# Optimization experiments

Hardware: AMD Instinct MI355X
Metric: run time of the kernel (lower is better)

The kernel has to match this reference:

```python
import jax, jax.numpy as jnp
import numpy as np

B, S, N, F, H = 128, 128, 24, 16, 32  # batch, seq, nodes, in-feat/node, hid/node


def setup_inputs() -> dict:
    key = jax.random.key(0)
    ks = jax.random.split(key, 7)
    IS, HS = N * F, N * H
    stdv = 1.0 / np.sqrt(HS).astype(np.float32)
    x = jax.random.normal(ks[0], (B, S, N, F), jnp.float32)
    h0 = jax.random.normal(ks[1], (B, N, H), jnp.float32)
    c0 = jax.random.normal(ks[2], (B, N, H), jnp.float32)
    G = jax.random.normal(ks[3], (N, N), jnp.float32)
    W = jax.random.uniform(ks[4], (IS, 4 * HS), jnp.float32, -stdv, stdv)
    U = jax.random.uniform(ks[5], (HS, 4 * HS), jnp.float32, -stdv, stdv)
    bias = jax.random.uniform(ks[6], (4 * HS,), jnp.float32, -stdv, stdv)
    return {"x": x, "h0": h0, "c0": c0, "W": W, "U": U, "bias": bias, "G": G}


def _graph_masks(G, F, H):
    # repeat_interleave(G, r, dim=-2) == kron(G, ones(r,1)); dim=-1 == kron(G, ones(1,c)).
    # Then tile x4 along last dim for the 4 LSTM gates.
    GW = jnp.tile(jnp.kron(G, jnp.ones((F, H), G.dtype)), (1, 4))  # [N*F, 4*N*H]
    GU = jnp.tile(jnp.kron(G, jnp.ones((H, H), G.dtype)), (1, 4))  # [N*H, 4*N*H]
    return GW, GU


def reference(x, h0, c0, W, U, bias, G):
    B, S, N, F = x.shape
    H = h0.shape[-1]
    HS = N * H
    GW, GU = _graph_masks(G, F, H)
    Wm = W * GW                      # masked input weights
    Um = U * GU                      # masked recurrent weights
    # Non-recurrent term batched into one big GEMM over all timesteps.
    xf = x.reshape(B, S, N * F)
    xg = jnp.einsum('bsi,ig->bsg', xf, Wm) + bias  # [B,S,4*HS]
    h = h0.reshape(B, HS)
    c = c0.reshape(B, HS)

    def step(carry, xg_t):
        h, c = carry
        gates = xg_t + h @ Um
        i = jax.nn.sigmoid(gates[:, :HS])
        f = jax.nn.sigmoid(gates[:, HS:2 * HS])
        g = jnp.tanh(gates[:, 2 * HS:3 * HS])
        o = jax.nn.sigmoid(gates[:, 3 * HS:])
        c = f * c + i * g
        h = o * jnp.tanh(c)
        return (h, c), h

    (h, c), hs = jax.lax.scan(step, (h, c), jnp.swapaxes(xg, 0, 1))  # hs: [S,B,HS]
    hidden_seq = jnp.swapaxes(hs, 0, 1).reshape(B, S, N, H)
    return hidden_seq, (h.reshape(B, N, H), c.reshape(B, N, H))
```

## Files before the change

### kernel.cpp

```cpp
#include <hip/hip_runtime.h>
#include <hip/hip_bf16.h>


typedef __bf16 bf16x8 __attribute__((ext_vector_type(8)));
typedef float f32x4 __attribute__((ext_vector_type(4)));

#define HS 768
#define GATES 3072
#define KV 1152
#define SEQ 128
#define BATCH 128
#define OUT_HID (BATCH*SEQ*HS)
#define LROW 2352
#define XOFF 768
#define NWG 192
#define TEAM_WGS 24

__device__ __forceinline__ float fast_sig(float x) {
    return 1.0f / (1.0f + __expf(-x));
}
__device__ __forceinline__ float fast_tanh(float x) {
    x = fminf(fmaxf(x, -15.0f), 15.0f);
    float e = __expf(2.0f * x);
    return (e - 1.0f) / (e + 1.0f);
}

__device__ __forceinline__ bf16x8 cvt8(const float* src) {
    float4 v0 = *(const float4*)src;
    float4 v1 = *(const float4*)(src + 4);
    bf16x8 p;
    p[0] = (__bf16)v0.x; p[1] = (__bf16)v0.y; p[2] = (__bf16)v0.z; p[3] = (__bf16)v0.w;
    p[4] = (__bf16)v1.x; p[5] = (__bf16)v1.y; p[6] = (__bf16)v1.z; p[7] = (__bf16)v1.w;
    return p;
}

__global__ void prep_kernel(const float* __restrict__ W, const float* __restrict__ U,
                            const float* __restrict__ G, __bf16* __restrict__ VmT) {
    __shared__ __bf16 tile[64][65];
    const int kvb = blockIdx.x * 64;
    const int cb  = blockIdx.y * 64;
    const int tid = threadIdx.x;
    {
        const int cl = tid & 63, kl0 = tid >> 6;
        #pragma unroll
        for (int i = 0; i < 16; ++i) {
            int kl = kl0 + i * 4;
            int kv = kvb + kl;
            int c  = cb + cl;
            int nout = (c % HS) >> 5;
            float g, v;
            if (kv < 384) {
                g = G[(kv >> 4) * 24 + nout];
                v = W[(size_t)kv * GATES + c];
            } else {
                int ku = kv - 384;
                g = G[(ku >> 5) * 24 + nout];
                v = U[(size_t)ku * GATES + c];
            }
            tile[kl][cl] = (__bf16)(v * g);
        }
    }
    __syncthreads();
    {
        const int kl = tid & 63, cl0 = tid >> 6;
        #pragma unroll
        for (int i = 0; i < 16; ++i) {
            int c = cl0 + i * 4;
            VmT[(size_t)(cb + c) * KV + kvb + kl] = tile[kl][c];
        }
    }
}

__global__ void prep_x(const float* __restrict__ x, __bf16* __restrict__ xb) {
    const int g = blockIdx.x * 256 + threadIdx.x;
    const int e = g * 8;
    const int b = e / (SEQ * 384);
    const int rem = e - b * (SEQ * 384);
    const int t = rem / 384;
    const int k = rem - t * 384;
    *(bf16x8*)&xb[((size_t)t * BATCH + b) * 384 + k] = cvt8(&x[e]);
}

__global__ __launch_bounds__(256, 1) void scan_kernel(
        const __bf16* __restrict__ xb,
        const float* __restrict__ h0,
        const float* __restrict__ c0,
        const __bf16* __restrict__ VmT,
        const float* __restrict__ bias,
        float* out,
        unsigned* xh32,
        unsigned* bar) {
    __shared__ __align__(16) char Bs[16 * LROW];
    const int tid = threadIdx.x;
    const int lane = tid & 63, wv = tid >> 6;
    const int m = lane & 15, quad = lane >> 4;
    const int team = blockIdx.x & 7, wg = blockIdx.x >> 3;
    const int bbase = team * 16;
    const int jbase = wg * 32 + wv * 8;

    unsigned* flags = bar;
    unsigned* myflag = flags + (team * TEAM_WGS + wg) * 16;

    bf16x8 w[2][36];
    #pragma unroll
    for (int T = 0; T < 2; ++T) {
        const int cg = (m & 3) * HS + jbase + 2 * (m >> 2) + T;
        const __bf16* wp = VmT + (size_t)cg * KV;
        #pragma unroll
        for (int kk = 0; kk < 36; ++kk)
            w[T][kk] = *(const bf16x8*)(wp + kk * 32 + quad * 8);
    }

    const int b_own = bbase + m;
    const int j0 = jbase + 2 * quad;
    const int j1 = j0 + 1;
    float cv0 = c0[b_own * HS + j0];
    float cv1 = c0[b_own * HS + j1];
    f32x4 bias0, bias1;
    #pragma unroll
    for (int r = 0; r < 4; ++r) {
        bias0[r] = bias[r * HS + j0];
        bias1[r] = bias[r * HS + j1];
    }

    #pragma unroll
    for (int i = 0; i < 3; ++i) {
        int ch = tid + i * 256;
        int row = ch / 48, c8 = ch % 48;
        *(uint4*)(Bs + row * LROW + c8 * 16) =
            *(const uint4*)&xb[((size_t)0 * BATCH + bbase + row) * 384 + c8 * 8];
    }
    #pragma unroll
    for (int i = 0; i < 6; ++i) {
        int ch = tid + i * 256;
        int row = ch / 96, c8h = ch % 96;
        bf16x8 p = cvt8(&h0[(size_t)(bbase + row) * HS + c8h * 8]);
        *(bf16x8*)(Bs + row * LROW + XOFF + c8h * 16) = p;
    }
    __syncthreads();

    #pragma unroll 1
    for (int t = 0; t < SEQ; ++t) {
        f32x4 acc0 = bias0, acc1 = bias1;
        const char* bfrag = Bs + m * LROW + quad * 16;
        #pragma unroll
        for (int kk = 0; kk < 36; ++kk) {
            bf16x8 bf = *(const bf16x8*)(bfrag + kk * 64);
            acc0 = __builtin_amdgcn_mfma_f32_16x16x32_bf16(w[0][kk], bf, acc0, 0, 0, 0);
            acc1 = __builtin_amdgcn_mfma_f32_16x16x32_bf16(w[1][kk], bf, acc1, 0, 0, 0);
        }

        float h0v, h1v;
        {
            float ii = fast_sig(acc0[0]), ff = fast_sig(acc0[1]);
            float gg = fast_tanh(acc0[2]), oo = fast_sig(acc0[3]);
            cv0 = ff * cv0 + ii * gg;
            h0v = oo * fast_tanh(cv0);
        }
        {
            float ii = fast_sig(acc1[0]), ff = fast_sig(acc1[1]);
            float gg = fast_tanh(acc1[2]), oo = fast_sig(acc1[3]);
            cv1 = ff * cv1 + ii * gg;
            h1v = oo * fast_tanh(cv1);
        }

        if (t == SEQ - 1) {
            const size_t obase = ((size_t)b_own * SEQ + t) * HS;
            *(float2*)&out[obase + j0] = make_float2(h0v, h1v);
            *(float2*)&out[OUT_HID + b_own * HS + j0] = make_float2(h0v, h1v);
            *(float2*)&out[OUT_HID + BATCH * HS + b_own * HS + j0] = make_float2(cv0, cv1);
            break;
        }

        {
            unsigned lo = (unsigned)__builtin_bit_cast(unsigned short, (__bf16)h0v);
            unsigned hi = (unsigned)__builtin_bit_cast(unsigned short, (__bf16)h1v);
            unsigned* dst = xh32 + ((size_t)(t & 1) * BATCH + b_own) * 384
                                 + (jbase >> 1) + quad;
            __hip_atomic_store(dst, lo | (hi << 16), __ATOMIC_RELAXED,
                               __HIP_MEMORY_SCOPE_AGENT);
        }
        {
            const size_t obase = ((size_t)b_own * SEQ + t) * HS;
            *(float2*)&out[obase + j0] = make_float2(h0v, h1v);
        }

        __syncthreads();

        if (tid == 0)
            __hip_atomic_store(myflag, (unsigned)(t + 1), __ATOMIC_RELAXED,
                               __HIP_MEMORY_SCOPE_AGENT);

        #pragma unroll
        for (int i = 0; i < 3; ++i) {
            int ch = tid + i * 256;
            int row = ch / 48, c8 = ch % 48;
            *(uint4*)(Bs + row * LROW + c8 * 16) =
                *(const uint4*)&xb[((size_t)(t + 1) * BATCH + bbase + row) * 384 + c8 * 8];
        }

        if (wv == 0 && lane < TEAM_WGS) {
            const unsigned* fp = flags + (team * TEAM_WGS + lane) * 16;
            while (__hip_atomic_load(fp, __ATOMIC_RELAXED,
                                     __HIP_MEMORY_SCOPE_AGENT) < (unsigned)(t + 1)) {
            }
        }
        __syncthreads();

        {
            const unsigned long long* src64 =
                (const unsigned long long*)xh32 + (size_t)(t & 1) * BATCH * 192;
            unsigned long long v[12];
            #pragma unroll
            for (int i = 0; i < 12; ++i) {
                int g = tid + i * 256;
                int row = g / 192, du = g % 192;
                v[i] = __hip_atomic_load(&src64[(size_t)(bbase + row) * 192 + du],
                                         __ATOMIC_RELAXED, __HIP_MEMORY_SCOPE_AGENT);
            }
            #pragma unroll
            for (int i = 0; i < 12; ++i) {
                int g = tid + i * 256;
                int row = g / 192, du = g % 192;
                *(unsigned long long*)(Bs + row * LROW + XOFF + du * 8) = v[i];
            }
        }
        __syncthreads();
    }
}

extern "C" void kernel_launch(void* const* d_in, const int* in_sizes, int n_in,
                              void* d_out, int out_size, void* d_ws, size_t ws_size,
                              hipStream_t stream) {
    (void)in_sizes; (void)n_in; (void)out_size; (void)ws_size;
    const float* x    = (const float*)d_in[0];
    const float* h0   = (const float*)d_in[1];
    const float* c0   = (const float*)d_in[2];
    const float* W    = (const float*)d_in[3];
    const float* U    = (const float*)d_in[4];
    const float* bias = (const float*)d_in[5];
    const float* G    = (const float*)d_in[6];
    float* out = (float*)d_out;

    char* wsb = (char*)d_ws;
    unsigned* bar = (unsigned*)wsb;
    __bf16* VmT  = (__bf16*)(wsb + 16384);
    __bf16* xb   = (__bf16*)(wsb + 16384 + (size_t)GATES * KV * 2);
    unsigned* xh32 = (unsigned*)(wsb + 16384 + (size_t)GATES * KV * 2
                                      + (size_t)SEQ * BATCH * 384 * 2);

    hipMemsetAsync(bar, 0, 16384, stream);
    prep_kernel<<<dim3(18, 48), 256, 0, stream>>>(W, U, G, VmT);
    prep_x<<<dim3(3072), 256, 0, stream>>>(x, xb);
    scan_kernel<<<dim3(NWG), dim3(256), 0, stream>>>(xb, h0, c0, VmT, bias,
                                                     out, xh32, bar);
}
```

Baseline: 580.3 us.

## Precompute input-projection MFMAs for next step while waiting on team barrier

Splits the per-step GEMM into an input part (x·W, 12 k-chunks) and a recurrent part (h·U, 24 k-chunks). The input contribution for step t+1 is computed right after step t's flag store, before the spin-wait on peer workgroups, using a double-buffered x tile in LDS that is prefetched two steps ahead. This takes work off the serial critical path between the barrier and the gate activation. The per-step output store is also moved after the flag signal. The cost is a larger LDS row and extra accumulator registers.

Result: no change. 573.3 us (-1.2%).

```diff
diff --git a/kernel.cpp b/kernel.cpp
--- a/kernel.cpp
+++ b/kernel.cpp
@@ -11,8 +11,8 @@
 #define SEQ 128
 #define BATCH 128
 #define OUT_HID (BATCH*SEQ*HS)
-#define LROW 2352
-#define XOFF 768
+#define LROW 3120
+#define HOFF 1536
 #define NWG 192
 #define TEAM_WGS 24
 
@@ -129,25 +129,38 @@
         int row = ch / 48, c8 = ch % 48;
         *(uint4*)(Bs + row * LROW + c8 * 16) =
             *(const uint4*)&xb[((size_t)0 * BATCH + bbase + row) * 384 + c8 * 8];
+        *(uint4*)(Bs + row * LROW + 768 + c8 * 16) =
+            *(const uint4*)&xb[((size_t)1 * BATCH + bbase + row) * 384 + c8 * 8];
     }
     #pragma unroll
     for (int i = 0; i < 6; ++i) {
         int ch = tid + i * 256;
         int row = ch / 96, c8h = ch % 96;
         bf16x8 p = cvt8(&h0[(size_t)(bbase + row) * HS + c8h * 8]);
-        *(bf16x8*)(Bs + row * LROW + XOFF + c8h * 16) = p;
+        *(bf16x8*)(Bs + row * LROW + HOFF + c8h * 16) = p;
     }
     __syncthreads();
+
+    f32x4 accA0 = bias0, accA1 = bias1;
+    {
+        const char* xf = Bs + m * LROW + quad * 16;
+        #pragma unroll
+        for (int kk = 0; kk < 12; ++kk) {
+            bf16x8 bf = *(const bf16x8*)(xf + kk * 64);
+            accA0 = __builtin_amdgcn_mfma_f32_16x16x32_bf16(w[0][kk], bf, accA0, 0, 0, 0);
+            accA1 = __builtin_amdgcn_mfma_f32_16x16x32_bf16(w[1][kk], bf, accA1, 0, 0, 0);
+        }
+    }
 
     #pragma unroll 1
     for (int t = 0; t < SEQ; ++t) {
-        f32x4 acc0 = bias0, acc1 = bias1;
-        const char* bfrag = Bs + m * LROW + quad * 16;
-        #pragma unroll
-        for (int kk = 0; kk < 36; ++kk) {
-            bf16x8 bf = *(const bf16x8*)(bfrag + kk * 64);
-            acc0 = __builtin_amdgcn_mfma_f32_16x16x32_bf16(w[0][kk], bf, acc0, 0, 0, 0);
-            acc1 = __builtin_amdgcn_mfma_f32_16x16x32_bf16(w[1][kk], bf, acc1, 0, 0, 0);
+        f32x4 acc0 = accA0, acc1 = accA1;
+        const char* hf = Bs + m * LROW + HOFF + quad * 16;
+        #pragma unroll
+        for (int p = 0; p < 24; ++p) {
+            bf16x8 bf = *(const bf16x8*)(hf + p * 64);
+            acc0 = __builtin_amdgcn_mfma_f32_16x16x32_bf16(w[0][12 + p], bf, acc0, 0, 0, 0);
+            acc1 = __builtin_amdgcn_mfma_f32_16x16x32_bf16(w[1][12 + p], bf, acc1, 0, 0, 0);
         }
 
         float h0v, h1v;
@@ -180,10 +193,6 @@
             __hip_atomic_store(dst, lo | (hi << 16), __ATOMIC_RELAXED,
                                __HIP_MEMORY_SCOPE_AGENT);
         }
-        {
-            const size_t obase = ((size_t)b_own * SEQ + t) * HS;
-            *(float2*)&out[obase + j0] = make_float2(h0v, h1v);
-        }
 
         __syncthreads();
 
@@ -191,12 +200,31 @@
             __hip_atomic_store(myflag, (unsigned)(t + 1), __ATOMIC_RELAXED,
                                __HIP_MEMORY_SCOPE_AGENT);
 
-        #pragma unroll
-        for (int i = 0; i < 3; ++i) {
-            int ch = tid + i * 256;
-            int row = ch / 48, c8 = ch % 48;
-            *(uint4*)(Bs + row * LROW + c8 * 16) =
-                *(const uint4*)&xb[((size_t)(t + 1) * BATCH + bbase + row) * 384 + c8 * 8];
+        {
+            const size_t obase = ((size_t)b_own * SEQ + t) * HS;
+            *(float2*)&out[obase + j0] = make_float2(h0v, h1v);
+        }
+
+        accA0 = bias0; accA1 = bias1;
+        {
+            const char* xf = Bs + m * LROW + (((t + 1) & 1) ? 768 : 0) + quad * 16;
+            #pragma unroll
+            for (int kk = 0; kk < 12; ++kk) {
+                bf16x8 bf = *(const bf16x8*)(xf + kk * 64);
+                accA0 = __builtin_amdgcn_mfma_f32_16x16x32_bf16(w[0][kk], bf, accA0, 0, 0, 0);
+                accA1 = __builtin_amdgcn_mfma_f32_16x16x32_bf16(w[1][kk], bf, accA1, 0, 0, 0);
+            }
+        }
+
+        if (t + 2 < SEQ) {
+            const int xoff = (t & 1) ? 768 : 0;
+            #pragma unroll
+            for (int i = 0; i < 3; ++i) {
+                int ch = tid + i * 256;
+                int row = ch / 48, c8 = ch % 48;
+                *(uint4*)(Bs + row * LROW + xoff + c8 * 16) =
+                    *(const uint4*)&xb[((size_t)(t + 2) * BATCH + bbase + row) * 384 + c8 * 8];
+            }
         }
 
         if (wv == 0 && lane < TEAM_WGS) {
@@ -222,7 +250,7 @@
             for (int i = 0; i < 12; ++i) {
                 int g = tid + i * 256;
                 int row = g / 192, du = g % 192;
-                *(unsigned long long*)(Bs + row * LROW + XOFF + du * 8) = v[i];
+                *(unsigned long long*)(Bs + row * LROW + HOFF + du * 8) = v[i];
             }
         }
         __syncthreads();
```
